# Optimization experiments

Measured on AMD Instinct MI355X. Metric: run time of the kernel, lower is better.

## Reference

```python
import jax, jax.numpy as jnp
import numpy as np

D_MODEL = 96
D_STATE = 16
D_INNER = 192   # expand * d_model
DT_RANK = 6     # ceil(96/16)
D_DEPTH_OUT = 1024  # (64/2)*(64/2)
BATCH, HH, WW = 2, 64, 64


def silu(v):
    return v * jax.nn.sigmoid(v)


def setup_inputs() -> dict:
    key = jax.random.key(0)
    ks = jax.random.split(key, 10)
    f = jnp.float32
    x = jax.random.normal(ks[0], (BATCH, HH, WW, D_MODEL), f)
    in_proj_w = jax.random.normal(ks[1], (2 * D_INNER, D_MODEL), f) * 0.02
    conv2d_w = jax.random.normal(ks[2], (D_INNER, 1, 3, 3), f) * 0.1  # depthwise, groups=D_INNER
    conv2d_b = jnp.zeros((D_INNER,), f)
    depth_conv_w = jax.random.normal(ks[3], (D_INNER, 1, 3, 3), f) * 0.1  # depthwise, stride 2
    depth_conv_b = jnp.zeros((D_INNER,), f)
    depth_fc_w = jax.random.normal(ks[4], (D_INNER, D_DEPTH_OUT), f) * 0.02
    depth_fc_b = jnp.zeros((D_INNER,), f)
    x_proj_w = jax.random.normal(ks[5], (DT_RANK + 2 * D_STATE, D_INNER), f) * 0.02
    dt_init_std = DT_RANK ** (-0.5)
    dt_projs_w = jax.random.uniform(ks[6], (D_INNER, DT_RANK), f, -dt_init_std, dt_init_std)
    # inverse-softplus of dt ~ U(log 1e-3, log 0.1)
    dt = jnp.exp(jax.random.uniform(ks[7], (D_INNER,), f) * (np.log(0.1) - np.log(0.001)) + np.log(0.001))
    dt = jnp.clip(dt, 1e-4, None)
    dt_projs_b = dt + jnp.log(-jnp.expm1(-dt))
    A_logs = jnp.log(jnp.tile(jnp.arange(1, D_STATE + 1, dtype=f)[None, :], (D_INNER, 1)))
    Ds = jnp.ones((D_INNER,), f)
    out_norm_w = jnp.ones((D_INNER,), f)
    out_norm_b = jnp.zeros((D_INNER,), f)
    out_proj_w = jax.random.normal(ks[8], (D_MODEL, D_INNER), f) * 0.02
    return dict(x=x, in_proj_w=in_proj_w, conv2d_w=conv2d_w, conv2d_b=conv2d_b,
                depth_conv_w=depth_conv_w, depth_conv_b=depth_conv_b,
                depth_fc_w=depth_fc_w, depth_fc_b=depth_fc_b, x_proj_w=x_proj_w,
                dt_projs_w=dt_projs_w, dt_projs_b=dt_projs_b, A_logs=A_logs, Ds=Ds,
                out_norm_w=out_norm_w, out_norm_b=out_norm_b, out_proj_w=out_proj_w)


def _selective_scan(u, delta, A, Bm, Cm, D, delta_bias):
    # u, delta: [B, D, L]; A: [D, N]; Bm, Cm: [B, N, L]; D: [D]; delta_bias: [D]
    delta = jax.nn.softplus(delta + delta_bias[None, :, None])
    dA = jnp.exp(jnp.einsum('bdl,dn->lbdn', delta, A))          # [L,B,D,N]
    dBu = jnp.einsum('bdl,bnl,bdl->lbdn', delta, Bm, u)          # [L,B,D,N]
    Ct = jnp.transpose(Cm, (2, 0, 1))                            # [L,B,N]
    h0 = jnp.zeros(dA.shape[1:], u.dtype)

    def step(h, inp):
        a, b, c = inp
        h = a * h + b                                            # S6 recurrence
        return h, jnp.einsum('bdn,bn->bd', h, c)

    _, ys = jax.lax.scan(step, h0, (dA, dBu, Ct))                # ys: [L,B,D]
    y = jnp.transpose(ys, (1, 2, 0))                             # [B,D,L]
    return y + D[None, :, None] * u


def _forward(x, in_proj_w, conv2d_w, conv2d_b, depth_conv_w, depth_conv_b,
             depth_fc_w, depth_fc_b, x_proj_w, dt_projs_w, dt_projs_b,
             A_logs, Ds, out_norm_w, out_norm_b, out_proj_w):
    B, H, W, _ = x.shape
    Di, N, R = D_INNER, D_STATE, DT_RANK
    dn = ('NCHW', 'OIHW', 'NCHW')
    xz = x @ in_proj_w.T
    x1, z = jnp.split(xz, 2, axis=-1)
    xc = jnp.transpose(x1, (0, 3, 1, 2))                         # [B,Di,H,W]
    xc = jax.lax.conv_general_dilated(xc, conv2d_w, (1, 1), [(1, 1), (1, 1)],
                                      dimension_numbers=dn, feature_group_count=Di)
    xc = silu(xc + conv2d_b[None, :, None, None])
    dxc = jax.lax.conv_general_dilated(xc, depth_conv_w, (2, 2), [(1, 1), (1, 1)],
                                       dimension_numbers=dn, feature_group_count=Di)
    dxc = dxc + depth_conv_b[None, :, None, None]                # [B,Di,H/2,W/2]
    dx = dxc.reshape(B, Di, -1)                                  # [B,Di,1024]
    dx = dx @ depth_fc_w.T + depth_fc_b                          # [B,Di,Di]
    dx = silu(jnp.transpose(dx, (0, 2, 1)))                      # [B,Di,CC], CC=Di
    L = H * W
    CC = dx.shape[-1]
    xs = jnp.concatenate([dx, xc.reshape(B, Di, L)], axis=-1)    # mode='head': [B,Di,LL]
    x_dbl = jnp.einsum('bdl,cd->bcl', xs, x_proj_w)
    dts, Bm, Cm = x_dbl[:, :R], x_dbl[:, R:R + N], x_dbl[:, R + N:]
    dts = jnp.einsum('brl,dr->bdl', dts, dt_projs_w)
    A = -jnp.exp(A_logs)
    y = _selective_scan(xs, dts, A, Bm, Cm, Ds, dt_projs_b)
    y = y[..., CC:]                                              # drop depth tokens (head mode)
    y = jnp.transpose(y, (0, 2, 1)).reshape(B, H, W, Di)
    mu = jnp.mean(y, axis=-1, keepdims=True)
    var = jnp.var(y, axis=-1, keepdims=True)
    y = (y - mu) * jax.lax.rsqrt(var + 1e-5) * out_norm_w + out_norm_b
    y = y * silu(z)
    return y @ out_proj_w.T


def reference(x, in_proj_w, conv2d_w, conv2d_b, depth_conv_w, depth_conv_b,
              depth_fc_w, depth_fc_b, x_proj_w, dt_projs_w, dt_projs_b,
              A_logs, Ds, out_norm_w, out_norm_b, out_proj_w):
    return _forward(x, in_proj_w, conv2d_w, conv2d_b, depth_conv_w, depth_conv_b,
                    depth_fc_w, depth_fc_b, x_proj_w, dt_projs_w, dt_projs_b,
                    A_logs, Ds, out_norm_w, out_norm_b, out_proj_w)
```

## Files before the change

### kernel.cpp

```cpp
#include <hip/hip_runtime.h>
#include <hip/hip_bf16.h>

typedef __hip_bfloat16 bf16;

#define BATCH 2
#define DM 96
#define DI 192
#define LSP 4096
#define LD 192
#define LTOT 4288
#define NST 16
#define RK 6
#define DFC 1024
#define CLEN 64
#define NCH 67
#define SCH 64
#define XR 16
#define NG  (BATCH * DI * NST)

__device__ __forceinline__ float b2f(bf16 v) { return __bfloat162float(v); }
__device__ __forceinline__ float silu_f(float x) { return x / (1.f + __expf(-x)); }
__device__ __forceinline__ float softplus_f(float x) { return x > 20.f ? x : log1pf(__expf(x)); }

__device__ __forceinline__ int is_f32(const void* alog) {
    return ((const unsigned int*)alog)[0] == 0u;
}
__device__ __forceinline__ float LDI(const void* p, int i, int f32m) {
    return f32m ? ((const float*)p)[i] : __bfloat162float(((const bf16*)p)[i]);
}
__device__ __forceinline__ void unpack2(unsigned int u, float* o) {
    o[0] = __uint_as_float(u << 16);
    o[1] = __uint_as_float(u & 0xffff0000u);
}

__device__ __forceinline__ float row16_sum(float v) {
    v += __int_as_float(__builtin_amdgcn_update_dpp(0, __float_as_int(v), 0x128, 0xf, 0xf, true));
    v += __int_as_float(__builtin_amdgcn_update_dpp(0, __float_as_int(v), 0x124, 0xf, 0xf, true));
    v += __int_as_float(__builtin_amdgcn_update_dpp(0, __float_as_int(v), 0x122, 0xf, 0xf, true));
    v += __int_as_float(__builtin_amdgcn_update_dpp(0, __float_as_int(v), 0x121, 0xf, 0xf, true));
    return v;
}

#define TW(r, i)  ((r) * 64 + ((((i) >> 2) + (r)) & 15) * 4 + ((i) & 3))

__global__ __launch_bounds__(256) void k_wprep(const void* __restrict__ ipw, float* __restrict__ wT,
                                               const void* __restrict__ alog) {
    const int f32m = is_f32(alog);
    int idx = blockIdx.x * 256 + threadIdx.x;
    if (idx < 96 * 384) {
        int k = idx / 384, c = idx - k * 384;
        wT[idx] = LDI(ipw, c * 96 + k, f32m);
    }
}

__global__ __launch_bounds__(384) void k_inproj2(const void* __restrict__ x, const float* __restrict__ wT,
                                                 float* __restrict__ x1, float* __restrict__ z,
                                                 const void* __restrict__ alog) {
    __shared__ __align__(16) float sx[16 * 100];
    const int f32m = is_f32(alog);
    int t = threadIdx.x;
    int row0 = blockIdx.x * 16;
    {
        int e = t * 4;
        int row = e / 96, k = e - row * 96;
        float4 v;
        if (f32m) {
            v = *((const float4*)((const float*)x + (row0 + row) * 96 + k));
        } else {
            uint2 u = *((const uint2*)((const ushort*)x + (row0 + row) * 96 + k));
            float f[4];
            unpack2(u.x, &f[0]); unpack2(u.y, &f[2]);
            v = make_float4(f[0], f[1], f[2], f[3]);
        }
        *(float4*)&sx[row * 100 + k] = v;
    }
    __syncthreads();
    int rg = t / 96, cg = t - rg * 96;
    int c0 = cg * 4, rbase = rg * 4;
    float acc[4][4];
    #pragma unroll
    for (int r = 0; r < 4; r++)
        #pragma unroll
        for (int cc = 0; cc < 4; cc++) acc[r][cc] = 0.f;
    const float* wp = wT + c0;
    #pragma unroll 4
    for (int k4 = 0; k4 < 24; k4++) {
        float4 xv[4], wv[4];
        #pragma unroll
        for (int r = 0; r < 4; r++) xv[r] = *(const float4*)&sx[(rbase + r) * 100 + k4 * 4];
        #pragma unroll
        for (int q = 0; q < 4; q++) wv[q] = *(const float4*)&wp[(k4 * 4 + q) * 384];
        #pragma unroll
        for (int r = 0; r < 4; r++) {
            float xr[4] = {xv[r].x, xv[r].y, xv[r].z, xv[r].w};
            #pragma unroll
            for (int q = 0; q < 4; q++) {
                acc[r][0] += xr[q] * wv[q].x;
                acc[r][1] += xr[q] * wv[q].y;
                acc[r][2] += xr[q] * wv[q].z;
                acc[r][3] += xr[q] * wv[q].w;
            }
        }
    }
    #pragma unroll
    for (int r = 0; r < 4; r++) {
        int row = row0 + rbase + r;
        float4 o = make_float4(acc[r][0], acc[r][1], acc[r][2], acc[r][3]);
        if (c0 < DI) *(float4*)&x1[row * DI + c0] = o;
        else         *(float4*)&z[row * DI + (c0 - DI)] = o;
    }
}

__global__ __launch_bounds__(192) void k_conv1(const float* __restrict__ x1, const void* __restrict__ cw,
                                               const void* __restrict__ cb, float* __restrict__ xs,
                                               const void* __restrict__ alog) {
    const int f32m = is_f32(alog);
    int d = threadIdx.x;
    int blk = blockIdx.x;
    int b = blk >> 9;
    int rest = blk & 511;
    int h = rest >> 3, w0 = (rest & 7) * 8;
    float wgt[9];
    #pragma unroll
    for (int i = 0; i < 9; i++) wgt[i] = LDI(cw, d * 9 + i, f32m);
    float bias = LDI(cb, d, f32m);
    float val[3][10];
    #pragma unroll
    for (int dh = 0; dh < 3; dh++) {
        int hh = h + dh - 1;
        #pragma unroll
        for (int j = 0; j < 10; j++) {
            int ww = w0 + j - 1;
            val[dh][j] = ((unsigned)hh < 64u && (unsigned)ww < 64u)
                       ? x1[((b << 12) + (hh << 6) + ww) * DI + d] : 0.f;
        }
    }
    #pragma unroll
    for (int i = 0; i < 8; i++) {
        float acc = bias;
        #pragma unroll
        for (int dh = 0; dh < 3; dh++)
            #pragma unroll
            for (int dw = 0; dw < 3; dw++)
                acc += val[dh][i + dw] * wgt[dh * 3 + dw];
        xs[(b * LTOT + LD + (h << 6) + w0 + i) * DI + d] = silu_f(acc);
    }
}

__global__ __launch_bounds__(192) void k_conv2(const float* __restrict__ xs, const void* __restrict__ dw,
                                               const void* __restrict__ db, float* __restrict__ dxc,
                                               const void* __restrict__ alog) {
    const int f32m = is_f32(alog);
    int d = threadIdx.x;
    int blk = blockIdx.x;
    int b = blk >> 10, lp = blk & 1023;
    int hp = lp >> 5, wp = lp & 31;
    float acc = LDI(db, d, f32m);
    #pragma unroll
    for (int dh = 0; dh < 3; dh++) {
        int h = 2 * hp + dh - 1;
        if ((unsigned)h >= 64u) continue;
        #pragma unroll
        for (int dw_ = 0; dw_ < 3; dw_++) {
            int w_ = 2 * wp + dw_ - 1;
            if ((unsigned)w_ >= 64u) continue;
            acc += xs[(b * LTOT + LD + (h << 6) + w_) * DI + d] * LDI(dw, d * 9 + dh * 3 + dw_, f32m);
        }
    }
    dxc[(b * DFC + lp) * DI + d] = acc;
}

__global__ __launch_bounds__(192) void k_dfc(const float* __restrict__ dxc, const void* __restrict__ fw,
                                             float* __restrict__ part, const void* __restrict__ alog) {
    __shared__ float sfw[4 * 128];
    const int f32m = is_f32(alog);
    int t = threadIdx.x;
    int blk = blockIdx.x;
    int p = blk / 96;
    int rem = blk - p * 96;
    int b   = rem / 48;
    int ch0 = (rem % 48) * 4;
    int k0  = p * 128;
    for (int idx = t; idx < 4 * 128; idx += 192)
        sfw[idx] = LDI(fw, (ch0 + (idx >> 7)) * DFC + k0 + (idx & 127), f32m);
    __syncthreads();
    float a0 = 0.f, a1 = 0.f, a2 = 0.f, a3 = 0.f;
    #pragma unroll 8
    for (int k = 0; k < 128; k++) {
        float dv = dxc[(b * DFC + k0 + k) * DI + t];
        a0 += dv * sfw[k];
        a1 += dv * sfw[128 + k];
        a2 += dv * sfw[256 + k];
        a3 += dv * sfw[384 + k];
    }
    int ob = ((p * 2 + b) * 192 + t) * DI + ch0;
    *(float4*)&part[ob] = make_float4(a0, a1, a2, a3);
}

__global__ __launch_bounds__(256) void k_xdbl(const float* __restrict__ xs_r, float* __restrict__ xs_w,
                                              const float* __restrict__ part, const void* __restrict__ fb,
                                              const void* __restrict__ xpw,
                                              float* __restrict__ BCb, float* __restrict__ dts,
                                              const void* __restrict__ alog) {
    __shared__ float sw[38 * 196];
    __shared__ float srow[XR][196];
    const int f32m = is_f32(alog);
    int t = threadIdx.x;
    for (int c = t >> 3; c < 38; c += 32) {
        int seg = (t & 7) * 24;
        for (int k = seg; k < seg + 24; k++) sw[c * 196 + k] = LDI(xpw, c * DI + k, f32m);
    }
    int row0 = blockIdx.x * XR;
    int bb = row0 >= LTOT ? 1 : 0;
    int depth = (row0 - bb * LTOT) < LD;
    for (int idx = t; idx < XR * DI; idx += 256) {
        int row = idx / DI, k = idx - row * DI;
        int grow = row0 + row;
        float v;
        if (depth) {
            int tok = grow - bb * LTOT;
            int o = (bb * 192 + tok) * DI + k;
            v = 0.f;
            #pragma unroll
            for (int p = 0; p < 8; p++) v += part[o + p * 73728];
            v = silu_f(v + LDI(fb, k, f32m));
            xs_w[grow * DI + k] = v;
        } else {
            v = xs_r[grow * DI + k];
        }
        srow[row][k] = v;
    }
    __syncthreads();
    int r = t & 15, cg = t >> 4;
    float a0 = 0.f, a1 = 0.f, a2 = 0.f;
    const float4* w0 = (const float4*)&sw[cg * 196];
    const float4* w1 = (const float4*)&sw[(cg + 16) * 196];
    const float4* w2 = (const float4*)&sw[(cg < 6 ? cg + 32 : cg) * 196];
    const float4* xr = (const float4*)&srow[r][0];
    #pragma unroll 4
    for (int k = 0; k < 48; k++) {
        float4 xv = xr[k], v0 = w0[k], v1 = w1[k], v2 = w2[k];
        a0 += xv.x * v0.x + xv.y * v0.y + xv.z * v0.z + xv.w * v0.w;
        a1 += xv.x * v1.x + xv.y * v1.y + xv.z * v1.z + xv.w * v1.w;
        a2 += xv.x * v2.x + xv.y * v2.y + xv.z * v2.z + xv.w * v2.w;
    }
    int grow = row0 + r;
    if (cg < 6) dts[grow * 6 + cg] = a0;
    else        BCb[grow * 32 + (cg - 6)] = a0;
    BCb[grow * 32 + (cg + 10)] = a1;
    if (cg < 6) BCb[grow * 32 + (cg + 26)] = a2;
}

__device__ __forceinline__ void delta_block_T(const float* sdts, const float* sdwb, float* sdel, int t) {
    int e = t * 4;
    int i = e >> 4, dl = e & 15;
    #pragma unroll
    for (int q = 0; q < 4; q++) {
        int r = dl + q;
        float dv = sdwb[96 + r];
        #pragma unroll
        for (int r2 = 0; r2 < RK; r2++) dv += sdts[i * RK + r2] * sdwb[r * RK + r2];
        sdel[TW(r, i)] = softplus_f(dv);
    }
}

__global__ __launch_bounds__(256) void k_scan1(const float* __restrict__ dts, const float* __restrict__ xs,
                                               const float* __restrict__ BCb, const void* __restrict__ dtw,
                                               const void* __restrict__ dtb, const void* __restrict__ alog,
                                               float2* __restrict__ AH) {
    __shared__ __align__(16) float su[1024];
    __shared__ __align__(16) float sB[1024];
    __shared__ __align__(16) float sdel[1024];
    __shared__ float sdts[CLEN * RK];
    __shared__ float sdwb[112];
    const int f32m = is_f32(alog);
    int t = threadIdx.x;
    int beta = blockIdx.x;
    int b = beta / (12 * NCH);
    int rem = beta - b * (12 * NCH);
    int dblk = rem / NCH, ch = rem - dblk * NCH;
    int d0 = dblk * 16, l0 = ch * CLEN;
    int bL = b * LTOT;
    {
        int e = t * 4;
        int i = e >> 4, dd = e & 15;
        float4 uv = *(const float4*)&xs[(bL + l0 + i) * DI + d0 + dd];
        float4 bv = *(const float4*)&BCb[(bL + l0 + i) * 32 + dd];
        float uu[4] = {uv.x, uv.y, uv.z, uv.w};
        float vb[4] = {bv.x, bv.y, bv.z, bv.w};
        #pragma unroll
        for (int q = 0; q < 4; q++) {
            int w = TW(dd + q, i);
            su[w] = uu[q];
            sB[w] = vb[q];
        }
    }
    for (int idx = t; idx < CLEN * RK; idx += 256) sdts[idx] = dts[(bL + l0) * RK + idx];
    if (t < 96)            sdwb[t] = LDI(dtw, (d0 + t / 6) * RK + (t % 6), f32m);
    else if (t < 112)      sdwb[t] = LDI(dtb, d0 + (t - 96), f32m);
    __syncthreads();
    delta_block_T(sdts, sdwb, sdel, t);
    __syncthreads();
    int dloc = t >> 4, n = t & 15;
    int d = d0 + dloc;
    float A = -__expf(LDI(alog, d * NST + n, f32m));
    float h = 0.f, ap = 1.f;
    int bd = dloc * 64, bn = n * 64;
    #pragma unroll
    for (int i4 = 0; i4 < 16; i4++) {
        int od = bd + (((i4 + dloc) & 15) << 2);
        int on = bn + (((i4 + n) & 15) << 2);
        float de[4], uu[4], vb[4];
        *(float4*)de = *(const float4*)&sdel[od];
        *(float4*)uu = *(const float4*)&su[od];
        *(float4*)vb = *(const float4*)&sB[on];
        #pragma unroll
        for (int q = 0; q < 4; q++) {
            float a = __expf(de[q] * A);
            h = a * h + de[q] * vb[q] * uu[q];
            ap *= a;
        }
    }
    int g = ((b * DI + d) * NST) + n;
    AH[ch * NG + g] = make_float2(ap, h);
}

__global__ __launch_bounds__(64) void k_scan2(const float2* __restrict__ AH, float* __restrict__ He) {
    int g = blockIdx.x * 64 + threadIdx.x;
    float h = 0.f;
    for (int ch = 0; ch < NCH; ch++) {
        He[ch * NG + g] = h;
        float2 v = AH[ch * NG + g];
        h = v.x * h + v.y;
    }
}

__global__ __launch_bounds__(256) void k_scan3(const float* __restrict__ dts, const float* __restrict__ xs,
                                               const float* __restrict__ BCb, const void* __restrict__ dtw,
                                               const void* __restrict__ dtb, const void* __restrict__ alog,
                                               const void* __restrict__ Dsv, const float* __restrict__ He,
                                               float* __restrict__ y) {
    __shared__ __align__(16) float su[1024];
    __shared__ __align__(16) float sbc[2048];
    __shared__ __align__(16) float sdel[1024];
    __shared__ float sdts[CLEN * RK];
    __shared__ float sdwb[112];
    const int f32m = is_f32(alog);
    int t = threadIdx.x;
    int beta = blockIdx.x;
    int b = beta / (12 * SCH);
    int rem = beta - b * (12 * SCH);
    int dblk = rem / SCH, ch = (rem - dblk * SCH) + 3;
    int d0 = dblk * 16, l0 = ch * CLEN;
    int bL = b * LTOT;
    {
        int e = t * 4;
        int i = e >> 4, dd = e & 15;
        float4 uv = *(const float4*)&xs[(bL + l0 + i) * DI + d0 + dd];
        float uu[4] = {uv.x, uv.y, uv.z, uv.w};
        #pragma unroll
        for (int q = 0; q < 4; q++) su[TW(dd + q, i)] = uu[q];
    }
    #pragma unroll
    for (int q2 = 0; q2 < 2; q2++) {
        int e = (t + q2 * 256) * 4;
        int i = e >> 5, c = e & 31;
        float4 v = *(const float4*)&BCb[(bL + l0 + i) * 32 + c];
        float vv[4] = {v.x, v.y, v.z, v.w};
        #pragma unroll
        for (int q = 0; q < 4; q++) sbc[TW(c + q, i)] = vv[q];
    }
    for (int idx = t; idx < CLEN * RK; idx += 256) sdts[idx] = dts[(bL + l0) * RK + idx];
    if (t < 96)            sdwb[t] = LDI(dtw, (d0 + t / 6) * RK + (t % 6), f32m);
    else if (t < 112)      sdwb[t] = LDI(dtb, d0 + (t - 96), f32m);
    __syncthreads();
    delta_block_T(sdts, sdwb, sdel, t);
    __syncthreads();
    int dloc = t >> 4, n = t & 15;
    int d = d0 + dloc;
    float A = -__expf(LDI(alog, d * NST + n, f32m));
    float Dv = LDI(Dsv, d, f32m);
    int g = ((b * DI + d) * NST) + n;
    float h = He[ch * NG + g];
    int bd = dloc * 64, bn = n * 64;
    #pragma unroll
    for (int i4 = 0; i4 < 16; i4++) {
        int od = bd + (((i4 + dloc) & 15) << 2);
        int on = bn + (((i4 + n) & 15) << 2);
        float de[4], uu[4], vb[4], vc[4];
        *(float4*)de = *(const float4*)&sdel[od];
        *(float4*)uu = *(const float4*)&su[od];
        *(float4*)vb = *(const float4*)&sbc[on];
        *(float4*)vc = *(const float4*)&sbc[on + 1024];
        #pragma unroll
        for (int q = 0; q < 4; q++) {
            float a = __expf(de[q] * A);
            h = a * h + de[q] * vb[q] * uu[q];
            float yv = row16_sum(h * vc[q]);
            if (n == 0) {
                int l = l0 + i4 * 4 + q;
                y[(b * LSP + (l - LD)) * DI + d] = yv + Dv * uu[q];
            }
        }
    }
}

__global__ __launch_bounds__(384) void k_out(const float* __restrict__ y, const float* __restrict__ z,
                                             const void* __restrict__ nw, const void* __restrict__ nb,
                                             const void* __restrict__ opw, void* __restrict__ out,
                                             const void* __restrict__ alog) {
    __shared__ float sg[2][DI];
    __shared__ float sred[2][2][3];
    const int f32m = is_f32(alog);
    int t = threadIdx.x;
    int m = t >> 2, kh = t & 3;
    float wr[48];
    if (f32m) {
        const float4* wp = (const float4*)((const float*)opw + m * DI + kh * 48);
        #pragma unroll
        for (int i = 0; i < 12; i++) {
            float4 v = wp[i];
            wr[4*i] = v.x; wr[4*i+1] = v.y; wr[4*i+2] = v.z; wr[4*i+3] = v.w;
        }
    } else {
        const uint4* wp = (const uint4*)((const bf16*)opw + m * DI + kh * 48);
        #pragma unroll
        for (int i = 0; i < 6; i++) {
            uint4 v = wp[i];
            unpack2(v.x, &wr[8*i]);   unpack2(v.y, &wr[8*i+2]);
            unpack2(v.z, &wr[8*i+4]); unpack2(v.w, &wr[8*i+6]);
        }
    }
    float nwv = 0.f, nbv = 0.f;
    if (t < DI) { nwv = LDI(nw, t, f32m); nbv = LDI(nb, t, f32m); }
    int wv_ = t >> 6;
    int row0 = blockIdx.x * 16;
    for (int pr = 0; pr < 8; pr++) {
        int r0 = row0 + pr * 2, r1 = r0 + 1;
        float y0 = 0.f, z0 = 0.f, y1 = 0.f, z1 = 0.f;
        if (t < DI) {
            y0 = y[r0 * DI + t]; z0 = z[r0 * DI + t];
            y1 = y[r1 * DI + t]; z1 = z[r1 * DI + t];
            float s0 = y0, q0 = y0 * y0, s1 = y1, q1 = y1 * y1;
            #pragma unroll
            for (int off = 32; off; off >>= 1) {
                s0 += __shfl_xor(s0, off); q0 += __shfl_xor(q0, off);
                s1 += __shfl_xor(s1, off); q1 += __shfl_xor(q1, off);
            }
            if ((t & 63) == 0) {
                sred[0][0][wv_] = s0; sred[0][1][wv_] = q0;
                sred[1][0][wv_] = s1; sred[1][1][wv_] = q1;
            }
        }
        __syncthreads();
        if (t < DI) {
            float S0  = sred[0][0][0] + sred[0][0][1] + sred[0][0][2];
            float Q0  = sred[0][1][0] + sred[0][1][1] + sred[0][1][2];
            float S1  = sred[1][0][0] + sred[1][0][1] + sred[1][0][2];
            float Q1  = sred[1][1][0] + sred[1][1][1] + sred[1][1][2];
            float mu0 = S0 * (1.f / 192.f), var0 = Q0 * (1.f / 192.f) - mu0 * mu0;
            float mu1 = S1 * (1.f / 192.f), var1 = Q1 * (1.f / 192.f) - mu1 * mu1;
            float g0 = (y0 - mu0) * rsqrtf(var0 + 1e-5f) * nwv + nbv;
            g0 *= z0 / (1.f + __expf(-z0));
            float g1 = (y1 - mu1) * rsqrtf(var1 + 1e-5f) * nwv + nbv;
            g1 *= z1 / (1.f + __expf(-z1));
            sg[0][t] = g0;
            sg[1][t] = g1;
        }
        __syncthreads();
        const float* g0p = &sg[0][kh * 48];
        const float* g1p = &sg[1][kh * 48];
        float a0 = 0.f, a1 = 0.f;
        #pragma unroll
        for (int j = 0; j < 48; j++) {
            a0 += g0p[j] * wr[j];
            a1 += g1p[j] * wr[j];
        }
        a0 += __shfl_xor(a0, 1); a0 += __shfl_xor(a0, 2);
        a1 += __shfl_xor(a1, 1); a1 += __shfl_xor(a1, 2);
        if (kh == 0) {
            if (f32m) {
                ((float*)out)[r0 * DM + m] = a0;
                ((float*)out)[r1 * DM + m] = a1;
            } else {
                ((bf16*)out)[r0 * DM + m] = __float2bfloat16(a0);
                ((bf16*)out)[r1 * DM + m] = __float2bfloat16(a1);
            }
        }
    }
}

extern "C" void kernel_launch(void* const* d_in, const int* in_sizes, int n_in,
                              void* d_out, int out_size, void* d_ws, size_t ws_size,
                              hipStream_t stream) {
    (void)in_sizes; (void)n_in; (void)out_size; (void)ws_size;
    const void* x    = d_in[0];
    const void* ipw  = d_in[1];
    const void* c1w  = d_in[2];
    const void* c1b  = d_in[3];
    const void* c2w  = d_in[4];
    const void* c2b  = d_in[5];
    const void* fcw  = d_in[6];
    const void* fcb  = d_in[7];
    const void* xpw  = d_in[8];
    const void* dtw  = d_in[9];
    const void* dtb  = d_in[10];
    const void* alog = d_in[11];
    const void* Dsv  = d_in[12];
    const void* nw   = d_in[13];
    const void* nb   = d_in[14];
    const void* opw  = d_in[15];

    float* ws  = (float*)d_ws;
    float* x1  = ws;
    float* z   = x1  + BATCH * LSP * DI;
    float* xs  = z   + BATCH * LSP * DI;
    float* dxc = xs  + BATCH * LTOT * DI;
    float* BCb = dxc + BATCH * DFC * DI;
    float* dts = BCb + BATCH * LTOT * 32;
    float2* AH = (float2*)(dts + BATCH * LTOT * RK);
    float* He  = (float*)(AH + NCH * NG);
    float* wT  = He + NCH * NG;
    float* part = x1;
    float* y    = x1;

    k_wprep  <<<dim3(144), dim3(256), 0, stream>>>(ipw, wT, alog);
    k_inproj2<<<dim3(512), dim3(384), 0, stream>>>(x, wT, x1, z, alog);
    k_conv1  <<<dim3(1024), dim3(DI), 0, stream>>>(x1, c1w, c1b, xs, alog);
    k_conv2  <<<dim3(BATCH * DFC), dim3(DI), 0, stream>>>(xs, c2w, c2b, dxc, alog);
    k_dfc    <<<dim3(768), dim3(DI), 0, stream>>>(dxc, fcw, part, alog);
    k_xdbl   <<<dim3(536), dim3(256), 0, stream>>>(xs, xs, part, fcb, xpw, BCb, dts, alog);
    k_scan1  <<<dim3(BATCH * 12 * NCH), dim3(256), 0, stream>>>(dts, xs, BCb, dtw, dtb, alog, AH);
    k_scan2  <<<dim3(96), dim3(64), 0, stream>>>(AH, He);
    k_scan3  <<<dim3(BATCH * 12 * SCH), dim3(256), 0, stream>>>(dts, xs, BCb, dtw, dtb, alog, Dsv, He, y);
    k_out    <<<dim3(512), dim3(384), 0, stream>>>(y, z, nw, nb, opw, d_out, alog);
}
```

Measured before the change: 221.8 us.

## Fuse three-pass chunked scan into single-pass decoupled look-back scan

Replaces the three scan kernels (chunk aggregates, serial carry propagation, rescan) with a single kernel. Each block takes a per-chain ticket for its chunk index, publishes its aggregate, then looks back over earlier chunks' flags to get its carry-in before rescanning to produce outputs. This removes two kernel launches, the AH/He global round trip and the duplicate loads and delta computation done in the third pass. In exchange, blocks spin-wait on their predecessors across the device, and flags are reset in the weight-prep kernel.

```diff
diff --git a/kernel.cpp b/kernel.cpp
--- a/kernel.cpp
+++ b/kernel.cpp
@@ -14,9 +14,9 @@
 #define DFC 1024
 #define CLEN 64
 #define NCH 67
-#define SCH 64
 #define XR 16
-#define NG  (BATCH * DI * NST)
+#define NCHAIN (BATCH * 12)
+#define NFLAGS (NCHAIN * NCH)
 
 __device__ __forceinline__ float b2f(bf16 v) { return __bfloat162float(v); }
 __device__ __forceinline__ float silu_f(float x) { return x / (1.f + __expf(-x)); }
@@ -44,9 +44,10 @@
 #define TW(r, i)  ((r) * 64 + ((((i) >> 2) + (r)) & 15) * 4 + ((i) & 3))
 
 __global__ __launch_bounds__(256) void k_wprep(const void* __restrict__ ipw, float* __restrict__ wT,
-                                               const void* __restrict__ alog) {
+                                               const void* __restrict__ alog, int* __restrict__ flags) {
     const int f32m = is_f32(alog);
     int idx = blockIdx.x * 256 + threadIdx.x;
+    if (idx < NFLAGS + NCHAIN) flags[idx] = 0;
     if (idx < 96 * 384) {
         int k = idx / 384, c = idx - k * 384;
         wT[idx] = LDI(ipw, c * 96 + k, f32m);
@@ -264,36 +265,44 @@
     }
 }
 
-__global__ __launch_bounds__(256) void k_scan1(const float* __restrict__ dts, const float* __restrict__ xs,
+__global__ __launch_bounds__(256) void k_scanf(const float* __restrict__ dts, const float* __restrict__ xs,
                                                const float* __restrict__ BCb, const void* __restrict__ dtw,
                                                const void* __restrict__ dtb, const void* __restrict__ alog,
-                                               float2* __restrict__ AH) {
+                                               const void* __restrict__ Dsv,
+                                               float2* __restrict__ pubag, float* __restrict__ pubincl,
+                                               int* __restrict__ flags, int* __restrict__ tickets,
+                                               float* __restrict__ y) {
     __shared__ __align__(16) float su[1024];
-    __shared__ __align__(16) float sB[1024];
+    __shared__ __align__(16) float sbc[2048];
     __shared__ __align__(16) float sdel[1024];
     __shared__ float sdts[CLEN * RK];
     __shared__ float sdwb[112];
+    __shared__ int spos;
     const int f32m = is_f32(alog);
     int t = threadIdx.x;
-    int beta = blockIdx.x;
-    int b = beta / (12 * NCH);
-    int rem = beta - b * (12 * NCH);
-    int dblk = rem / NCH, ch = rem - dblk * NCH;
-    int d0 = dblk * 16, l0 = ch * CLEN;
+    int chain = blockIdx.x / NCH;
+    int b = chain / 12, dblk = chain - b * 12;
+    if (t == 0) spos = atomicAdd(&tickets[chain], 1);
+    __syncthreads();
+    int pos = spos;
+    int d0 = dblk * 16, l0 = pos * CLEN;
     int bL = b * LTOT;
     {
         int e = t * 4;
         int i = e >> 4, dd = e & 15;
         float4 uv = *(const float4*)&xs[(bL + l0 + i) * DI + d0 + dd];
-        float4 bv = *(const float4*)&BCb[(bL + l0 + i) * 32 + dd];
         float uu[4] = {uv.x, uv.y, uv.z, uv.w};
-        float vb[4] = {bv.x, bv.y, bv.z, bv.w};
-        #pragma unroll
-        for (int q = 0; q < 4; q++) {
-            int w = TW(dd + q, i);
-            su[w] = uu[q];
-            sB[w] = vb[q];
-        }
+        #pragma unroll
+        for (int q = 0; q < 4; q++) su[TW(dd + q, i)] = uu[q];
+    }
+    #pragma unroll
+    for (int q2 = 0; q2 < 2; q2++) {
+        int e = (t + q2 * 256) * 4;
+        int i = e >> 5, c = e & 31;
+        float4 v = *(const float4*)&BCb[(bL + l0 + i) * 32 + c];
+        float vv[4] = {v.x, v.y, v.z, v.w};
+        #pragma unroll
+        for (int q = 0; q < 4; q++) sbc[TW(c + q, i)] = vv[q];
     }
     for (int idx = t; idx < CLEN * RK; idx += 256) sdts[idx] = dts[(bL + l0) * RK + idx];
     if (t < 96)            sdwb[t] = LDI(dtw, (d0 + t / 6) * RK + (t % 6), f32m);
@@ -304,8 +313,8 @@
     int dloc = t >> 4, n = t & 15;
     int d = d0 + dloc;
     float A = -__expf(LDI(alog, d * NST + n, f32m));
+    int bd = dloc * 64, bn = n * 64;
     float h = 0.f, ap = 1.f;
-    int bd = dloc * 64, bn = n * 64;
     #pragma unroll
     for (int i4 = 0; i4 < 16; i4++) {
         int od = bd + (((i4 + dloc) & 15) << 2);
@@ -313,7 +322,7 @@
         float de[4], uu[4], vb[4];
         *(float4*)de = *(const float4*)&sdel[od];
         *(float4*)uu = *(const float4*)&su[od];
-        *(float4*)vb = *(const float4*)&sB[on];
+        *(float4*)vb = *(const float4*)&sbc[on];
         #pragma unroll
         for (int q = 0; q < 4; q++) {
             float a = __expf(de[q] * A);
@@ -321,68 +330,45 @@
             ap *= a;
         }
     }
-    int g = ((b * DI + d) * NST) + n;
-    AH[ch * NG + g] = make_float2(ap, h);
-}
-
-__global__ __launch_bounds__(64) void k_scan2(const float2* __restrict__ AH, float* __restrict__ He) {
-    int g = blockIdx.x * 64 + threadIdx.x;
-    float h = 0.f;
-    for (int ch = 0; ch < NCH; ch++) {
-        He[ch * NG + g] = h;
-        float2 v = AH[ch * NG + g];
-        h = v.x * h + v.y;
-    }
-}
-
-__global__ __launch_bounds__(256) void k_scan3(const float* __restrict__ dts, const float* __restrict__ xs,
-                                               const float* __restrict__ BCb, const void* __restrict__ dtw,
-                                               const void* __restrict__ dtb, const void* __restrict__ alog,
-                                               const void* __restrict__ Dsv, const float* __restrict__ He,
-                                               float* __restrict__ y) {
-    __shared__ __align__(16) float su[1024];
-    __shared__ __align__(16) float sbc[2048];
-    __shared__ __align__(16) float sdel[1024];
-    __shared__ float sdts[CLEN * RK];
-    __shared__ float sdwb[112];
-    const int f32m = is_f32(alog);
-    int t = threadIdx.x;
-    int beta = blockIdx.x;
-    int b = beta / (12 * SCH);
-    int rem = beta - b * (12 * SCH);
-    int dblk = rem / SCH, ch = (rem - dblk * SCH) + 3;
-    int d0 = dblk * 16, l0 = ch * CLEN;
-    int bL = b * LTOT;
-    {
-        int e = t * 4;
-        int i = e >> 4, dd = e & 15;
-        float4 uv = *(const float4*)&xs[(bL + l0 + i) * DI + d0 + dd];
-        float uu[4] = {uv.x, uv.y, uv.z, uv.w};
-        #pragma unroll
-        for (int q = 0; q < 4; q++) su[TW(dd + q, i)] = uu[q];
-    }
-    #pragma unroll
-    for (int q2 = 0; q2 < 2; q2++) {
-        int e = (t + q2 * 256) * 4;
-        int i = e >> 5, c = e & 31;
-        float4 v = *(const float4*)&BCb[(bL + l0 + i) * 32 + c];
-        float vv[4] = {v.x, v.y, v.z, v.w};
-        #pragma unroll
-        for (int q = 0; q < 4; q++) sbc[TW(c + q, i)] = vv[q];
-    }
-    for (int idx = t; idx < CLEN * RK; idx += 256) sdts[idx] = dts[(bL + l0) * RK + idx];
-    if (t < 96)            sdwb[t] = LDI(dtw, (d0 + t / 6) * RK + (t % 6), f32m);
-    else if (t < 112)      sdwb[t] = LDI(dtb, d0 + (t - 96), f32m);
-    __syncthreads();
-    delta_block_T(sdts, sdwb, sdel, t);
-    __syncthreads();
-    int dloc = t >> 4, n = t & 15;
-    int d = d0 + dloc;
-    float A = -__expf(LDI(alog, d * NST + n, f32m));
+    int slot = chain * NCH + pos;
+    pubag[slot * 256 + t] = make_float2(ap, h);
+    __syncthreads();
+    if (t == 0) __hip_atomic_store(&flags[slot], 1, __ATOMIC_RELEASE, __HIP_MEMORY_SCOPE_AGENT);
+    float h_in = 0.f;
+    if (pos > 0) {
+        float Acc = 1.f, Hc = 0.f;
+        int j = pos - 1;
+        while (true) {
+            int f;
+            do {
+                f = __hip_atomic_load(&flags[chain * NCH + j], __ATOMIC_ACQUIRE, __HIP_MEMORY_SCOPE_AGENT);
+                if (!f) __builtin_amdgcn_s_sleep(8);
+            } while (!f);
+            if (f == 2) {
+                float hi = __hip_atomic_load(&pubincl[(chain * NCH + j) * 256 + t],
+                                             __ATOMIC_RELAXED, __HIP_MEMORY_SCOPE_AGENT);
+                h_in = Hc + Acc * hi;
+                break;
+            }
+            unsigned long long agu = __hip_atomic_load(
+                (unsigned long long*)&pubag[(chain * NCH + j) * 256 + t],
+                __ATOMIC_RELAXED, __HIP_MEMORY_SCOPE_AGENT);
+            float agx = __uint_as_float((unsigned)(agu & 0xffffffffu));
+            float agy = __uint_as_float((unsigned)(agu >> 32));
+            Hc  = Hc + Acc * agy;
+            Acc = Acc * agx;
+            if (j == 0) { h_in = Hc; break; }
+            j--;
+        }
+    }
+    if (pos < NCH - 1) {
+        pubincl[slot * 256 + t] = ap * h_in + h;
+        __syncthreads();
+        if (t == 0) __hip_atomic_store(&flags[slot], 2, __ATOMIC_RELEASE, __HIP_MEMORY_SCOPE_AGENT);
+    }
+    if (pos < 3) return;
     float Dv = LDI(Dsv, d, f32m);
-    int g = ((b * DI + d) * NST) + n;
-    float h = He[ch * NG + g];
-    int bd = dloc * 64, bn = n * 64;
+    float h2 = h_in;
     #pragma unroll
     for (int i4 = 0; i4 < 16; i4++) {
         int od = bd + (((i4 + dloc) & 15) << 2);
@@ -395,8 +381,8 @@
         #pragma unroll
         for (int q = 0; q < 4; q++) {
             float a = __expf(de[q] * A);
-            h = a * h + de[q] * vb[q] * uu[q];
-            float yv = row16_sum(h * vc[q]);
+            h2 = a * h2 + de[q] * vb[q] * uu[q];
+            float yv = row16_sum(h2 * vc[q]);
             if (n == 0) {
                 int l = l0 + i4 * 4 + q;
                 y[(b * LSP + (l - LD)) * DI + d] = yv + Dv * uu[q];
@@ -518,20 +504,21 @@
     float* dxc = xs  + BATCH * LTOT * DI;
     float* BCb = dxc + BATCH * DFC * DI;
     float* dts = BCb + BATCH * LTOT * 32;
-    float2* AH = (float2*)(dts + BATCH * LTOT * RK);
-    float* He  = (float*)(AH + NCH * NG);
-    float* wT  = He + NCH * NG;
+    float2* pubag = (float2*)(dts + BATCH * LTOT * RK);
+    float* pubincl = (float*)(pubag + NFLAGS * 256);
+    int* flags   = (int*)(pubincl + NFLAGS * 256);
+    int* tickets = flags + NFLAGS;
+    float* wT  = (float*)(tickets + NCHAIN + 8);
     float* part = x1;
     float* y    = x1;
 
-    k_wprep  <<<dim3(144), dim3(256), 0, stream>>>(ipw, wT, alog);
+    k_wprep  <<<dim3(144), dim3(256), 0, stream>>>(ipw, wT, alog, flags);
     k_inproj2<<<dim3(512), dim3(384), 0, stream>>>(x, wT, x1, z, alog);
     k_conv1  <<<dim3(1024), dim3(DI), 0, stream>>>(x1, c1w, c1b, xs, alog);
     k_conv2  <<<dim3(BATCH * DFC), dim3(DI), 0, stream>>>(xs, c2w, c2b, dxc, alog);
     k_dfc    <<<dim3(768), dim3(DI), 0, stream>>>(dxc, fcw, part, alog);
     k_xdbl   <<<dim3(536), dim3(256), 0, stream>>>(xs, xs, part, fcb, xpw, BCb, dts, alog);
-    k_scan1  <<<dim3(BATCH * 12 * NCH), dim3(256), 0, stream>>>(dts, xs, BCb, dtw, dtb, alog, AH);
-    k_scan2  <<<dim3(96), dim3(64), 0, stream>>>(AH, He);
-    k_scan3  <<<dim3(BATCH * 12 * SCH), dim3(256), 0, stream>>>(dts, xs, BCb, dtw, dtb, alog, Dsv, He, y);
+    k_scanf  <<<dim3(NCHAIN * NCH), dim3(256), 0, stream>>>(dts, xs, BCb, dtw, dtb, alog, Dsv,
+                                                            pubag, pubincl, flags, tickets, y);
     k_out    <<<dim3(512), dim3(384), 0, stream>>>(y, z, nw, nb, opw, d_out, alog);
 }
```

Measured after the change: 741.5 us. +234.4%, slower.

## Fuse all pipeline stages into one cooperative persistent kernel with grid syncs

Applied to the files above, without the earlier changes.

Adds a single cooperative kernel that runs every stage (weight transpose, in-projection, convolutions, depth FC, x-projection, chunked scan passes, norm and out-projection) as grid-stride loops separated by grid-wide barriers. The grid size comes from the occupancy query and is cached. The goal is to remove per-kernel launch gaps and tail effects between the ten separate launches. In exchange, each stage runs at fixed 384-thread blocks with a large shared buffer, which may reduce occupancy, and each grid barrier costs time. The old multi-kernel path is kept as a fallback if the cooperative launch fails.

```diff
diff --git a/kernel.cpp b/kernel.cpp
--- a/kernel.cpp
+++ b/kernel.cpp
@@ -1,6 +1,8 @@
 #include <hip/hip_runtime.h>
+#include <hip/hip_cooperative_groups.h>
 #include <hip/hip_bf16.h>
 
+namespace cg = cooperative_groups;
 typedef __hip_bfloat16 bf16;
 
 #define BATCH 2
@@ -17,8 +19,8 @@
 #define SCH 64
 #define XR 16
 #define NG  (BATCH * DI * NST)
-
-__device__ __forceinline__ float b2f(bf16 v) { return __bfloat162float(v); }
+#define NTHR 384
+
 __device__ __forceinline__ float silu_f(float x) { return x / (1.f + __expf(-x)); }
 __device__ __forceinline__ float softplus_f(float x) { return x > 20.f ? x : log1pf(__expf(x)); }
 
@@ -42,6 +44,466 @@
 }
 
 #define TW(r, i)  ((r) * 64 + ((((i) >> 2) + (r)) & 15) * 4 + ((i) & 3))
+
+__device__ __forceinline__ void delta_block_T(const float* sdts, const float* sdwb, float* sdel, int t) {
+    int e = t * 4;
+    int i = e >> 4, dl = e & 15;
+    #pragma unroll
+    for (int q = 0; q < 4; q++) {
+        int r = dl + q;
+        float dv = sdwb[96 + r];
+        #pragma unroll
+        for (int r2 = 0; r2 < RK; r2++) dv += sdts[i * RK + r2] * sdwb[r * RK + r2];
+        sdel[TW(r, i)] = softplus_f(dv);
+    }
+}
+
+__global__ __launch_bounds__(NTHR) void k_mega(
+    const void* __restrict__ x,    const void* __restrict__ ipw,
+    const void* __restrict__ c1w,  const void* __restrict__ c1b,
+    const void* __restrict__ c2w,  const void* __restrict__ c2b,
+    const void* __restrict__ fcw,  const void* __restrict__ fcb,
+    const void* __restrict__ xpw,  const void* __restrict__ dtw,
+    const void* __restrict__ dtb,  const void* __restrict__ alog,
+    const void* __restrict__ Dsv,  const void* __restrict__ nw,
+    const void* __restrict__ nbv,  const void* __restrict__ opw,
+    void* __restrict__ out,        float* __restrict__ ws)
+{
+    cg::grid_group grid = cg::this_grid();
+    __shared__ __align__(16) float smem[10584];
+    const int f32m = is_f32(alog);
+    const int t = threadIdx.x;
+    const int nblk = gridDim.x;
+
+    float* x1  = ws;
+    float* z   = x1  + BATCH * LSP * DI;
+    float* xs  = z   + BATCH * LSP * DI;
+    float* dxc = xs  + BATCH * LTOT * DI;
+    float* BCb = dxc + BATCH * DFC * DI;
+    float* dts = BCb + BATCH * LTOT * 32;
+    float2* AH = (float2*)(dts + BATCH * LTOT * RK);
+    float* He  = (float*)(AH + NCH * NG);
+    float* wT  = He + NCH * NG;
+    float* part = x1;
+    float* y    = x1;
+
+    for (int idx = blockIdx.x * NTHR + t; idx < 96 * 384; idx += nblk * NTHR) {
+        int k = idx / 384, c = idx - k * 384;
+        wT[idx] = LDI(ipw, c * 96 + k, f32m);
+    }
+    grid.sync();
+
+    for (int vb = blockIdx.x; vb < 512; vb += nblk) {
+        int row0 = vb * 16;
+        {
+            int e = t * 4;
+            int row = e / 96, k = e - row * 96;
+            float4 v;
+            if (f32m) {
+                v = *((const float4*)((const float*)x + (row0 + row) * 96 + k));
+            } else {
+                uint2 u = *((const uint2*)((const ushort*)x + (row0 + row) * 96 + k));
+                float f[4];
+                unpack2(u.x, &f[0]); unpack2(u.y, &f[2]);
+                v = make_float4(f[0], f[1], f[2], f[3]);
+            }
+            *(float4*)&smem[row * 100 + k] = v;
+        }
+        __syncthreads();
+        int rg = t / 96, cgi = t - rg * 96;
+        int c0 = cgi * 4, rbase = rg * 4;
+        float acc[4][4];
+        #pragma unroll
+        for (int r = 0; r < 4; r++)
+            #pragma unroll
+            for (int cc = 0; cc < 4; cc++) acc[r][cc] = 0.f;
+        const float* wp = wT + c0;
+        #pragma unroll 4
+        for (int k4 = 0; k4 < 24; k4++) {
+            float4 xv[4], wv[4];
+            #pragma unroll
+            for (int r = 0; r < 4; r++) xv[r] = *(const float4*)&smem[(rbase + r) * 100 + k4 * 4];
+            #pragma unroll
+            for (int q = 0; q < 4; q++) wv[q] = *(const float4*)&wp[(k4 * 4 + q) * 384];
+            #pragma unroll
+            for (int r = 0; r < 4; r++) {
+                float xr[4] = {xv[r].x, xv[r].y, xv[r].z, xv[r].w};
+                #pragma unroll
+                for (int q = 0; q < 4; q++) {
+                    acc[r][0] += xr[q] * wv[q].x;
+                    acc[r][1] += xr[q] * wv[q].y;
+                    acc[r][2] += xr[q] * wv[q].z;
+                    acc[r][3] += xr[q] * wv[q].w;
+                }
+            }
+        }
+        #pragma unroll
+        for (int r = 0; r < 4; r++) {
+            int row = row0 + rbase + r;
+            float4 o = make_float4(acc[r][0], acc[r][1], acc[r][2], acc[r][3]);
+            if (c0 < DI) *(float4*)&x1[row * DI + c0] = o;
+            else         *(float4*)&z[row * DI + (c0 - DI)] = o;
+        }
+        __syncthreads();
+    }
+    grid.sync();
+
+    for (int vb = blockIdx.x; vb < 1024; vb += nblk) if (t < DI) {
+        int d = t;
+        int b = vb >> 9;
+        int rest = vb & 511;
+        int h = rest >> 3, w0 = (rest & 7) * 8;
+        float wgt[9];
+        #pragma unroll
+        for (int i = 0; i < 9; i++) wgt[i] = LDI(c1w, d * 9 + i, f32m);
+        float bias = LDI(c1b, d, f32m);
+        float val[3][10];
+        #pragma unroll
+        for (int dh = 0; dh < 3; dh++) {
+            int hh = h + dh - 1;
+            #pragma unroll
+            for (int j = 0; j < 10; j++) {
+                int ww = w0 + j - 1;
+                val[dh][j] = ((unsigned)hh < 64u && (unsigned)ww < 64u)
+                           ? x1[((b << 12) + (hh << 6) + ww) * DI + d] : 0.f;
+            }
+        }
+        #pragma unroll
+        for (int i = 0; i < 8; i++) {
+            float acc = bias;
+            #pragma unroll
+            for (int dh = 0; dh < 3; dh++)
+                #pragma unroll
+                for (int dw = 0; dw < 3; dw++)
+                    acc += val[dh][i + dw] * wgt[dh * 3 + dw];
+            xs[(b * LTOT + LD + (h << 6) + w0 + i) * DI + d] = silu_f(acc);
+        }
+    }
+    grid.sync();
+
+    for (int vb = blockIdx.x; vb < 2048; vb += nblk) if (t < DI) {
+        int d = t;
+        int b = vb >> 10, lp = vb & 1023;
+        int hp = lp >> 5, wp2 = lp & 31;
+        float acc = LDI(c2b, d, f32m);
+        #pragma unroll
+        for (int dh = 0; dh < 3; dh++) {
+            int h = 2 * hp + dh - 1;
+            if ((unsigned)h >= 64u) continue;
+            #pragma unroll
+            for (int dw_ = 0; dw_ < 3; dw_++) {
+                int w_ = 2 * wp2 + dw_ - 1;
+                if ((unsigned)w_ >= 64u) continue;
+                acc += xs[(b * LTOT + LD + (h << 6) + w_) * DI + d] * LDI(c2w, d * 9 + dh * 3 + dw_, f32m);
+            }
+        }
+        dxc[(b * DFC + lp) * DI + d] = acc;
+    }
+    grid.sync();
+
+    for (int vb = blockIdx.x; vb < 768; vb += nblk) {
+        int p = vb / 96;
+        int rem = vb - p * 96;
+        int b   = rem / 48;
+        int ch0 = (rem % 48) * 4;
+        int k0  = p * 128;
+        for (int idx = t; idx < 512; idx += NTHR)
+            smem[idx] = LDI(fcw, (ch0 + (idx >> 7)) * DFC + k0 + (idx & 127), f32m);
+        __syncthreads();
+        if (t < DI) {
+            float a0 = 0.f, a1 = 0.f, a2 = 0.f, a3 = 0.f;
+            #pragma unroll 8
+            for (int k = 0; k < 128; k++) {
+                float dv = dxc[(b * DFC + k0 + k) * DI + t];
+                a0 += dv * smem[k];
+                a1 += dv * smem[128 + k];
+                a2 += dv * smem[256 + k];
+                a3 += dv * smem[384 + k];
+            }
+            int ob = ((p * 2 + b) * 192 + t) * DI + ch0;
+            *(float4*)&part[ob] = make_float4(a0, a1, a2, a3);
+        }
+        __syncthreads();
+    }
+    grid.sync();
+
+    {
+        float* sw   = smem;
+        float* srow = smem + 38 * 196;
+        for (int c = t >> 3; c < 38; c += 48) {
+            int seg = (t & 7) * 24;
+            for (int k = seg; k < seg + 24; k++) sw[c * 196 + k] = LDI(xpw, c * DI + k, f32m);
+        }
+        for (int vb = blockIdx.x; vb < 536; vb += nblk) {
+            int row0 = vb * XR;
+            int bb = row0 >= LTOT ? 1 : 0;
+            int depth = (row0 - bb * LTOT) < LD;
+            for (int idx = t; idx < XR * DI; idx += NTHR) {
+                int row = idx / DI, k = idx - row * DI;
+                int grow = row0 + row;
+                float v;
+                if (depth) {
+                    int tok = grow - bb * LTOT;
+                    int o = (bb * 192 + tok) * DI + k;
+                    v = 0.f;
+                    #pragma unroll
+                    for (int p = 0; p < 8; p++) v += part[o + p * 73728];
+                    v = silu_f(v + LDI(fcb, k, f32m));
+                    xs[grow * DI + k] = v;
+                } else {
+                    v = xs[grow * DI + k];
+                }
+                srow[row * 196 + k] = v;
+            }
+            __syncthreads();
+            if (t < 256) {
+                int r = t & 15, cgi = t >> 4;
+                float a0 = 0.f, a1 = 0.f, a2 = 0.f;
+                const float4* w0 = (const float4*)&sw[cgi * 196];
+                const float4* w1 = (const float4*)&sw[(cgi + 16) * 196];
+                const float4* w2 = (const float4*)&sw[(cgi < 6 ? cgi + 32 : cgi) * 196];
+                const float4* xr = (const float4*)&srow[r * 196];
+                #pragma unroll 4
+                for (int k = 0; k < 48; k++) {
+                    float4 xv = xr[k], v0 = w0[k], v1 = w1[k], v2 = w2[k];
+                    a0 += xv.x * v0.x + xv.y * v0.y + xv.z * v0.z + xv.w * v0.w;
+                    a1 += xv.x * v1.x + xv.y * v1.y + xv.z * v1.z + xv.w * v1.w;
+                    a2 += xv.x * v2.x + xv.y * v2.y + xv.z * v2.z + xv.w * v2.w;
+                }
+                int grow = row0 + r;
+                if (cgi < 6) dts[grow * 6 + cgi] = a0;
+                else         BCb[grow * 32 + (cgi - 6)] = a0;
+                BCb[grow * 32 + (cgi + 10)] = a1;
+                if (cgi < 6) BCb[grow * 32 + (cgi + 26)] = a2;
+            }
+            __syncthreads();
+        }
+    }
+    grid.sync();
+
+    {
+        float* su   = smem;
+        float* sB   = smem + 1024;
+        float* sdel = smem + 2048;
+        float* sdts = smem + 3072;
+        float* sdwb = smem + 3456;
+        for (int vb = blockIdx.x; vb < BATCH * 12 * NCH; vb += nblk) {
+            int b = vb / (12 * NCH);
+            int rem = vb - b * (12 * NCH);
+            int dblk = rem / NCH, ch = rem - dblk * NCH;
+            int d0 = dblk * 16, l0 = ch * CLEN;
+            int bL = b * LTOT;
+            if (t < 256) {
+                int e = t * 4;
+                int i = e >> 4, dd = e & 15;
+                float4 uv = *(const float4*)&xs[(bL + l0 + i) * DI + d0 + dd];
+                float4 bv = *(const float4*)&BCb[(bL + l0 + i) * 32 + dd];
+                float uu[4] = {uv.x, uv.y, uv.z, uv.w};
+                float vbv[4] = {bv.x, bv.y, bv.z, bv.w};
+                #pragma unroll
+                for (int q = 0; q < 4; q++) {
+                    int w = TW(dd + q, i);
+                    su[w] = uu[q];
+                    sB[w] = vbv[q];
+                }
+            }
+            for (int idx = t; idx < CLEN * RK; idx += NTHR) sdts[idx] = dts[(bL + l0) * RK + idx];
+            if (t < 96)            sdwb[t] = LDI(dtw, (d0 + t / 6) * RK + (t % 6), f32m);
+            else if (t < 112)      sdwb[t] = LDI(dtb, d0 + (t - 96), f32m);
+            __syncthreads();
+            if (t < 256) delta_block_T(sdts, sdwb, sdel, t);
+            __syncthreads();
+            if (t < 256) {
+                int dloc = t >> 4, n = t & 15;
+                int d = d0 + dloc;
+                float A = -__expf(LDI(alog, d * NST + n, f32m));
+                float h = 0.f, ap = 1.f;
+                int bd = dloc * 64, bn = n * 64;
+                #pragma unroll
+                for (int i4 = 0; i4 < 16; i4++) {
+                    int od = bd + (((i4 + dloc) & 15) << 2);
+                    int on = bn + (((i4 + n) & 15) << 2);
+                    float de[4], uu[4], vbv[4];
+                    *(float4*)de  = *(const float4*)&sdel[od];
+                    *(float4*)uu  = *(const float4*)&su[od];
+                    *(float4*)vbv = *(const float4*)&sB[on];
+                    #pragma unroll
+                    for (int q = 0; q < 4; q++) {
+                        float a = __expf(de[q] * A);
+                        h = a * h + de[q] * vbv[q] * uu[q];
+                        ap *= a;
+                    }
+                }
+                int g = ((b * DI + d) * NST) + n;
+                AH[ch * NG + g] = make_float2(ap, h);
+            }
+            __syncthreads();
+        }
+    }
+    grid.sync();
+
+    for (int g = blockIdx.x * NTHR + t; g < NG; g += nblk * NTHR) {
+        float h = 0.f;
+        #pragma unroll 1
+        for (int ch = 0; ch < NCH; ch++) {
+            He[ch * NG + g] = h;
+            float2 v = AH[ch * NG + g];
+            h = v.x * h + v.y;
+        }
+    }
+    grid.sync();
+
+    {
+        float* su   = smem;
+        float* sbc  = smem + 1024;
+        float* sdel = smem + 3072;
+        float* sdts = smem + 4096;
+        float* sdwb = smem + 4480;
+        for (int vb = blockIdx.x; vb < BATCH * 12 * SCH; vb += nblk) {
+            int b = vb / (12 * SCH);
+            int rem = vb - b * (12 * SCH);
+            int dblk = rem / SCH, ch = (rem - dblk * SCH) + 3;
+            int d0 = dblk * 16, l0 = ch * CLEN;
+            int bL = b * LTOT;
+            if (t < 256) {
+                int e = t * 4;
+                int i = e >> 4, dd = e & 15;
+                float4 uv = *(const float4*)&xs[(bL + l0 + i) * DI + d0 + dd];
+                float uu[4] = {uv.x, uv.y, uv.z, uv.w};
+                #pragma unroll
+                for (int q = 0; q < 4; q++) su[TW(dd + q, i)] = uu[q];
+                #pragma unroll
+                for (int q2 = 0; q2 < 2; q2++) {
+                    int e2 = (t + q2 * 256) * 4;
+                    int i2 = e2 >> 5, c = e2 & 31;
+                    float4 v = *(const float4*)&BCb[(bL + l0 + i2) * 32 + c];
+                    float vv[4] = {v.x, v.y, v.z, v.w};
+                    #pragma unroll
+                    for (int q = 0; q < 4; q++) sbc[TW(c + q, i2)] = vv[q];
+                }
+            }
+            for (int idx = t; idx < CLEN * RK; idx += NTHR) sdts[idx] = dts[(bL + l0) * RK + idx];
+            if (t < 96)            sdwb[t] = LDI(dtw, (d0 + t / 6) * RK + (t % 6), f32m);
+            else if (t < 112)      sdwb[t] = LDI(dtb, d0 + (t - 96), f32m);
+            __syncthreads();
+            if (t < 256) delta_block_T(sdts, sdwb, sdel, t);
+            __syncthreads();
+            if (t < 256) {
+                int dloc = t >> 4, n = t & 15;
+                int d = d0 + dloc;
+                float A = -__expf(LDI(alog, d * NST + n, f32m));
+                float Dv = LDI(Dsv, d, f32m);
+                int g = ((b * DI + d) * NST) + n;
+                float h = He[ch * NG + g];
+                int bd = dloc * 64, bn = n * 64;
+                #pragma unroll
+                for (int i4 = 0; i4 < 16; i4++) {
+                    int od = bd + (((i4 + dloc) & 15) << 2);
+                    int on = bn + (((i4 + n) & 15) << 2);
+                    float de[4], uu[4], vbv[4], vc[4];
+                    *(float4*)de  = *(const float4*)&sdel[od];
+                    *(float4*)uu  = *(const float4*)&su[od];
+                    *(float4*)vbv = *(const float4*)&sbc[on];
+                    *(float4*)vc  = *(const float4*)&sbc[on + 1024];
+                    #pragma unroll
+                    for (int q = 0; q < 4; q++) {
+                        float a = __expf(de[q] * A);
+                        h = a * h + de[q] * vbv[q] * uu[q];
+                        float yv = row16_sum(h * vc[q]);
+                        if (n == 0) {
+                            int l = l0 + i4 * 4 + q;
+                            y[(b * LSP + (l - LD)) * DI + d] = yv + Dv * uu[q];
+                        }
+                    }
+                }
+            }
+            __syncthreads();
+        }
+    }
+    grid.sync();
+
+    {
+        float* sg   = smem;
+        float* sred = smem + 384;
+        int m = t >> 2, kh = t & 3;
+        float wr[48];
+        if (f32m) {
+            const float4* wp = (const float4*)((const float*)opw + m * DI + kh * 48);
+            #pragma unroll
+            for (int i = 0; i < 12; i++) {
+                float4 v = wp[i];
+                wr[4*i] = v.x; wr[4*i+1] = v.y; wr[4*i+2] = v.z; wr[4*i+3] = v.w;
+            }
+        } else {
+            const uint4* wp = (const uint4*)((const bf16*)opw + m * DI + kh * 48);
+            #pragma unroll
+            for (int i = 0; i < 6; i++) {
+                uint4 v = wp[i];
+                unpack2(v.x, &wr[8*i]);   unpack2(v.y, &wr[8*i+2]);
+                unpack2(v.z, &wr[8*i+4]); unpack2(v.w, &wr[8*i+6]);
+            }
+        }
+        float nwv = 0.f, nbvv = 0.f;
+        if (t < DI) { nwv = LDI(nw, t, f32m); nbvv = LDI(nbv, t, f32m); }
+        int wv_ = t >> 6;
+        for (int vb = blockIdx.x; vb < 512; vb += nblk) {
+            int row0 = vb * 16;
+            for (int pr = 0; pr < 8; pr++) {
+                int r0 = row0 + pr * 2, r1 = r0 + 1;
+                float y0 = 0.f, z0 = 0.f, y1 = 0.f, z1 = 0.f;
+                if (t < DI) {
+                    y0 = y[r0 * DI + t]; z0 = z[r0 * DI + t];
+                    y1 = y[r1 * DI + t]; z1 = z[r1 * DI + t];
+                    float s0 = y0, q0 = y0 * y0, s1 = y1, q1 = y1 * y1;
+                    #pragma unroll
+                    for (int off = 32; off; off >>= 1) {
+                        s0 += __shfl_xor(s0, off); q0 += __shfl_xor(q0, off);
+                        s1 += __shfl_xor(s1, off); q1 += __shfl_xor(q1, off);
+                    }
+                    if ((t & 63) == 0) {
+                        sred[(0*2+0)*3 + wv_] = s0; sred[(0*2+1)*3 + wv_] = q0;
+                        sred[(1*2+0)*3 + wv_] = s1; sred[(1*2+1)*3 + wv_] = q1;
+                    }
+                }
+                __syncthreads();
+                if (t < DI) {
+                    float S0 = sred[0] + sred[1] + sred[2];
+                    float Q0 = sred[3] + sred[4] + sred[5];
+                    float S1 = sred[6] + sred[7] + sred[8];
+                    float Q1 = sred[9] + sred[10] + sred[11];
+                    float mu0 = S0 * (1.f / 192.f), var0 = Q0 * (1.f / 192.f) - mu0 * mu0;
+                    float mu1 = S1 * (1.f / 192.f), var1 = Q1 * (1.f / 192.f) - mu1 * mu1;
+                    float g0 = (y0 - mu0) * rsqrtf(var0 + 1e-5f) * nwv + nbvv;
+                    g0 *= z0 / (1.f + __expf(-z0));
+                    float g1 = (y1 - mu1) * rsqrtf(var1 + 1e-5f) * nwv + nbvv;
+                    g1 *= z1 / (1.f + __expf(-z1));
+                    sg[t] = g0;
+                    sg[192 + t] = g1;
+                }
+                __syncthreads();
+                const float* g0p = &sg[kh * 48];
+                const float* g1p = &sg[192 + kh * 48];
+                float a0 = 0.f, a1 = 0.f;
+                #pragma unroll
+                for (int j = 0; j < 48; j++) {
+                    a0 += g0p[j] * wr[j];
+                    a1 += g1p[j] * wr[j];
+                }
+                a0 += __shfl_xor(a0, 1); a0 += __shfl_xor(a0, 2);
+                a1 += __shfl_xor(a1, 1); a1 += __shfl_xor(a1, 2);
+                if (kh == 0) {
+                    if (f32m) {
+                        ((float*)out)[r0 * DM + m] = a0;
+                        ((float*)out)[r1 * DM + m] = a1;
+                    } else {
+                        ((bf16*)out)[r0 * DM + m] = __float2bfloat16(a0);
+                        ((bf16*)out)[r1 * DM + m] = __float2bfloat16(a1);
+                    }
+                }
+            }
+        }
+    }
+}
 
 __global__ __launch_bounds__(256) void k_wprep(const void* __restrict__ ipw, float* __restrict__ wT,
                                                const void* __restrict__ alog) {
@@ -249,19 +711,6 @@
     else        BCb[grow * 32 + (cg - 6)] = a0;
     BCb[grow * 32 + (cg + 10)] = a1;
     if (cg < 6) BCb[grow * 32 + (cg + 26)] = a2;
-}
-
-__device__ __forceinline__ void delta_block_T(const float* sdts, const float* sdwb, float* sdel, int t) {
-    int e = t * 4;
-    int i = e >> 4, dl = e & 15;
-    #pragma unroll
-    for (int q = 0; q < 4; q++) {
-        int r = dl + q;
-        float dv = sdwb[96 + r];
-        #pragma unroll
-        for (int r2 = 0; r2 < RK; r2++) dv += sdts[i * RK + r2] * sdwb[r * RK + r2];
-        sdel[TW(r, i)] = softplus_f(dv);
-    }
 }
 
 __global__ __launch_bounds__(256) void k_scan1(const float* __restrict__ dts, const float* __restrict__ xs,
@@ -507,12 +956,28 @@
     const void* dtb  = d_in[10];
     const void* alog = d_in[11];
     const void* Dsv  = d_in[12];
-    const void* nw   = d_in[13];
-    const void* nb   = d_in[14];
+    const void* nwp  = d_in[13];
+    const void* nbp  = d_in[14];
     const void* opw  = d_in[15];
-
-    float* ws  = (float*)d_ws;
-    float* x1  = ws;
+    void* outp = d_out;
+    float* wsf = (float*)d_ws;
+
+    static int s_grid = 0;
+    if (s_grid == 0) {
+        int bpc = 0;
+        if (hipOccupancyMaxActiveBlocksPerMultiprocessor(&bpc, k_mega, NTHR, 0) != hipSuccess || bpc < 1)
+            bpc = 2;
+        if (bpc > 8) bpc = 8;
+        s_grid = bpc * 256;
+    }
+
+    void* kargs[18] = { &x, &ipw, &c1w, &c1b, &c2w, &c2b, &fcw, &fcb, &xpw,
+                        &dtw, &dtb, &alog, &Dsv, &nwp, &nbp, &opw, &outp, &wsf };
+    hipError_t err = hipLaunchCooperativeKernel((const void*)k_mega, dim3(s_grid), dim3(NTHR),
+                                                kargs, 0, stream);
+    if (err == hipSuccess) return;
+
+    float* x1  = wsf;
     float* z   = x1  + BATCH * LSP * DI;
     float* xs  = z   + BATCH * LSP * DI;
     float* dxc = xs  + BATCH * LTOT * DI;
@@ -533,5 +998,5 @@
     k_scan1  <<<dim3(BATCH * 12 * NCH), dim3(256), 0, stream>>>(dts, xs, BCb, dtw, dtb, alog, AH);
     k_scan2  <<<dim3(96), dim3(64), 0, stream>>>(AH, He);
     k_scan3  <<<dim3(BATCH * 12 * SCH), dim3(256), 0, stream>>>(dts, xs, BCb, dtw, dtb, alog, Dsv, He, y);
-    k_out    <<<dim3(512), dim3(384), 0, stream>>>(y, z, nw, nb, opw, d_out, alog);
-}
+    k_out    <<<dim3(512), dim3(384), 0, stream>>>(y, z, nwp, nbp, opw, outp, alog);
+}
```

Result: slower. 563.0 us (+153.9%).
